# Kernel optimization log

Hardware: AMD Instinct MI355X
Metric: run time of the kernel (lower is better)

Reference implementation:

```python
import jax, jax.numpy as jnp
import numpy as np

B, CHAR_LEN, LSTM, VOCAB, NATTN = 4096, 64, 400, 73, 10

def _lstm_cell(x, h, c, W_ih, W_hh, b):
    # gates: [B, 4*LSTM] in (i, f, g, o) order, matching torch.nn.LSTMCell
    g = x @ W_ih.T + h @ W_hh.T + b
    i, f, gg, o = jnp.split(g, 4, axis=1)
    i = jax.nn.sigmoid(i); f = jax.nn.sigmoid(f)
    gg = jnp.tanh(gg); o = jax.nn.sigmoid(o)
    c_new = f * c + i * gg
    h_new = o * jnp.tanh(c_new)
    return h_new, c_new

def setup_inputs() -> dict:
    key = jax.random.key(0)
    ks = jax.random.split(key, 24)
    d = {}
    d['inputs'] = jax.random.normal(ks[0], (B, 3), jnp.float32)
    for n, k in zip(['h1','c1','h2','c2','h3','c3'], ks[1:7]):
        d[n] = jax.random.normal(k, (B, LSTM), jnp.float32) * 0.1
    d['kappa'] = jax.random.uniform(ks[7], (B, NATTN), jnp.float32) * 5.0
    d['w_prev'] = jax.random.uniform(ks[8], (B, VOCAB), jnp.float32)
    d['attention_values'] = jax.random.uniform(ks[9], (B, CHAR_LEN, VOCAB), jnp.float32)
    d['attention_lengths'] = jax.random.randint(ks[10], (B,), 1, CHAR_LEN + 1, jnp.int32)
    s = 0.05
    in1 = VOCAB + 3              # lstm1 input: [w, inputs]
    in23 = 3 + LSTM + VOCAB      # lstm2/3 input: [inputs, h, w]
    attn_in = VOCAB + 3 + LSTM
    d['W_ih1'] = jax.random.normal(ks[11], (4 * LSTM, in1), jnp.float32) * s
    d['W_hh1'] = jax.random.normal(ks[12], (4 * LSTM, LSTM), jnp.float32) * s
    d['b1'] = jax.random.normal(ks[13], (4 * LSTM,), jnp.float32) * s
    d['W_attn'] = jax.random.normal(ks[14], (3 * NATTN, attn_in), jnp.float32) * s
    d['b_attn'] = jax.random.normal(ks[15], (3 * NATTN,), jnp.float32) * s
    d['W_ih2'] = jax.random.normal(ks[16], (4 * LSTM, in23), jnp.float32) * s
    d['W_hh2'] = jax.random.normal(ks[17], (4 * LSTM, LSTM), jnp.float32) * s
    d['b2'] = jax.random.normal(ks[18], (4 * LSTM,), jnp.float32) * s
    d['W_ih3'] = jax.random.normal(ks[19], (4 * LSTM, in23), jnp.float32) * s
    d['W_hh3'] = jax.random.normal(ks[20], (4 * LSTM, LSTM), jnp.float32) * s
    d['b3'] = jax.random.normal(ks[21], (4 * LSTM,), jnp.float32) * s
    return d

def reference(inputs, h1, c1, h2, c2, h3, c3, kappa, w_prev, attention_values,
              attention_lengths, W_ih1, W_hh1, b1, W_attn, b_attn,
              W_ih2, W_hh2, b2, W_ih3, W_hh3, b3):
    char_len = attention_values.shape[1]
    # --- LSTM 1 ---
    s1_in = jnp.concatenate([w_prev, inputs], axis=1)
    h1n, c1n = _lstm_cell(s1_in, h1, c1, W_ih1, W_hh1, b1)
    # --- Gaussian-mixture location attention ---
    attn_in = jnp.concatenate([w_prev, inputs, h1n], axis=1)
    attn_params = jax.nn.softplus(attn_in @ W_attn.T + b_attn)
    alpha, beta, kap = jnp.split(attn_params, 3, axis=1)
    kap = kappa + kap / 25.0
    beta = jnp.maximum(beta, 0.01)
    u = jnp.arange(char_len, dtype=jnp.float32)[None, None, :]           # [1,1,C]
    phi = jnp.sum(alpha[:, :, None] *
                  jnp.exp(-jnp.square(kap[:, :, None] - u) / beta[:, :, None]),
                  axis=1)                                                 # [B,C]
    seq_mask = (jnp.arange(char_len)[None, :] < attention_lengths[:, None]).astype(jnp.float32)
    w = jnp.einsum('bc,bcv->bv', phi * seq_mask, attention_values)        # [B,V]
    # --- LSTM 2 & 3 ---
    s2_in = jnp.concatenate([inputs, h1n, w], axis=1)
    h2n, c2n = _lstm_cell(s2_in, h2, c2, W_ih2, W_hh2, b2)
    s3_in = jnp.concatenate([inputs, h2n, w], axis=1)
    h3n, c3n = _lstm_cell(s3_in, h3, c3, W_ih3, W_hh3, b3)
    return h3n
```

## Files before the change

kernel.cpp:

```cpp
#include <hip/hip_runtime.h>
#include <hip/hip_bf16.h>


#define B_SZ     4096
#define LSTM_N   400
#define NG       1600
#define VOCAB    73
#define NATTN    10
#define CHARLEN  64
#define KP1      512
#define KP23     896

typedef _Float16 half8 __attribute__((ext_vector_type(8)));
typedef __attribute__((ext_vector_type(4))) float floatx4;

__device__ __forceinline__ void gload_lds16(const void* g, void* l) {
    __builtin_amdgcn_global_load_lds(
        (const __attribute__((address_space(1))) void*)g,
        (__attribute__((address_space(3))) void*)l, 16, 0, 0);
}

__device__ __forceinline__ int lds_off(int r, int g) {
    return (r << 6) + ((((g ^ r) & 7)) << 3);
}

__global__ __launch_bounds__(256) void pack_wall(const float* __restrict__ Wih1,
                                                 const float* __restrict__ Whh1,
                                                 const float* __restrict__ Wih2,
                                                 const float* __restrict__ Whh2,
                                                 const float* __restrict__ Wih3,
                                                 const float* __restrict__ Whh3,
                                                 const float* __restrict__ W_attn,
                                                 _Float16* __restrict__ W1,
                                                 _Float16* __restrict__ W2,
                                                 _Float16* __restrict__ W3,
                                                 _Float16* __restrict__ Wa)
{
    const int z = blockIdx.z;
    const int n = blockIdx.y;
    const int k = blockIdx.x * 256 + threadIdx.x;
    if (z == 3) {
        if (n >= 64 || k >= KP1) return;
        float v = (n < 30 && k < 476) ? W_attn[(size_t)n * 476 + k] : 0.f;
        Wa[(size_t)n * KP1 + k] = (_Float16)v;
        return;
    }
    if (n >= NG) return;
    const int u = n >> 2, g = n & 3;
    const int src = g * 400 + u;
    if (z == 0) {
        if (k >= KP1) return;
        float v = 0.f;
        if (k < 76)           v = Wih1[(size_t)src * 76 + k];
        else if (k < 476)     v = Whh1[(size_t)src * 400 + (k - 76)];
        W1[(size_t)n * KP1 + k] = (_Float16)v;
    } else {
        if (k >= KP23) return;
        const float* Wih = (z == 1) ? Wih2 : Wih3;
        const float* Whh = (z == 1) ? Whh2 : Whh3;
        float v = 0.f;
        if (k < 476)          v = Wih[(size_t)src * 476 + k];
        else if (k < 876)     v = Whh[(size_t)src * 400 + (k - 476)];
        ((z == 1) ? W2 : W3)[(size_t)n * KP23 + k] = (_Float16)v;
    }
}

__global__ __launch_bounds__(256) void pack_x(const float* __restrict__ w_prev,
                                              const float* __restrict__ inputs,
                                              const float* __restrict__ h1,
                                              const float* __restrict__ h2,
                                              const float* __restrict__ h3,
                                              _Float16* __restrict__ X1,
                                              _Float16* __restrict__ XA,
                                              _Float16* __restrict__ X2,
                                              _Float16* __restrict__ X3)
{
    const int b = blockIdx.y;
    const int k = blockIdx.x * 256 + threadIdx.x;
    if (k < KP1) {
        float v = 0.f;
        if (k < 73)        v = w_prev[(size_t)b * 73 + k];
        else if (k < 76)   v = inputs[(size_t)b * 3 + (k - 73)];
        else if (k < 476)  v = h1[(size_t)b * 400 + (k - 76)];
        X1[(size_t)b * KP1 + k] = (_Float16)v;
        if (k < 76 || k >= 476) XA[(size_t)b * KP1 + k] = (_Float16)v;
    }
    const int kk = k - KP1;
    if (kk >= 0 && kk < KP23) {
        if (kk >= 3 && kk < 476) return;
        float v2 = 0.f, v3 = 0.f;
        if (kk < 3) { v2 = inputs[(size_t)b * 3 + kk]; v3 = v2; }
        else if (kk >= 476 && kk < 876) {
            v2 = h2[(size_t)b * 400 + (kk - 476)];
            v3 = h3[(size_t)b * 400 + (kk - 476)];
        }
        X2[(size_t)b * KP23 + kk] = (_Float16)v2;
        X3[(size_t)b * KP23 + kk] = (_Float16)v3;
    }
}

__global__ __launch_bounds__(256) void gemm_fused(const _Float16* __restrict__ Wm,
                                                  const _Float16* __restrict__ X,
                                                  const float* __restrict__ bias,
                                                  const float* __restrict__ c_in,
                                                  _Float16* __restrict__ d1, int ld1,
                                                  _Float16* __restrict__ d2, int ld2,
                                                  float* __restrict__ fout, int Kp)
{
    __shared__ _Float16 As[64 * 64];
    __shared__ _Float16 Bs[128 * 64];

    const int t    = threadIdx.x;
    const int w    = t >> 6;
    const int lane = t & 63;
    const int quad = lane >> 4;
    const int l16  = lane & 15;
    const int m0   = blockIdx.y * 64;
    const int n0   = blockIdx.x * 128;
    const int wm   = (w >> 1) * 32;
    const int wn   = (w & 1) * 64;
    const int lr   = lane >> 3;
    const int gq   = (lane & 7) ^ lr;

    floatx4 acc[2][4] = {};

    for (int k0 = 0; k0 < Kp; k0 += 64) {
        __syncthreads();
        {
            const int cr = w * 16;
#pragma unroll
            for (int s = 0; s < 2; s++)
                gload_lds16(Wm + (size_t)(m0 + cr + s * 8 + lr) * Kp + k0 + gq * 8,
                            As + (cr + s * 8) * 64);
        }
#pragma unroll
        for (int j = 0; j < 2; j++) {
            const int cr = (j * 4 + w) * 16;
#pragma unroll
            for (int s = 0; s < 2; s++)
                gload_lds16(X + (size_t)(n0 + cr + s * 8 + lr) * Kp + k0 + gq * 8,
                            Bs + (cr + s * 8) * 64);
        }
        asm volatile("s_waitcnt vmcnt(0)" ::: "memory");
        __syncthreads();

#pragma unroll
        for (int h = 0; h < 2; h++) {
            half8 af[2], bf[4];
#pragma unroll
            for (int i = 0; i < 2; i++)
                af[i] = *(const half8*)(As + lds_off(wm + i * 16 + l16, h * 4 + quad));
#pragma unroll
            for (int i = 0; i < 4; i++)
                bf[i] = *(const half8*)(Bs + lds_off(wn + i * 16 + l16, h * 4 + quad));
#pragma unroll
            for (int mt = 0; mt < 2; mt++)
#pragma unroll
                for (int nt = 0; nt < 4; nt++)
                    acc[mt][nt] = __builtin_amdgcn_mfma_f32_16x16x32_f16(
                        af[mt], bf[nt], acc[mt][nt], 0, 0, 0);
        }
    }

#pragma unroll
    for (int mt = 0; mt < 2; mt++) {
        const int u = ((m0 + wm + mt * 16) >> 2) + quad;
        const float bi  = bias[u];
        const float bff = bias[400 + u];
        const float bg  = bias[800 + u];
        const float bo  = bias[1200 + u];
#pragma unroll
        for (int nt = 0; nt < 4; nt++) {
            const int b = n0 + wn + nt * 16 + l16;
            float gi = acc[mt][nt][0] + bi;
            float gf = acc[mt][nt][1] + bff;
            float gg = acc[mt][nt][2] + bg;
            float go = acc[mt][nt][3] + bo;
            float si = 1.f / (1.f + expf(-gi));
            float sf = 1.f / (1.f + expf(-gf));
            float so = 1.f / (1.f + expf(-go));
            float cn = sf * c_in[(size_t)b * LSTM_N + u] + si * tanhf(gg);
            float h  = so * tanhf(cn);
            if (fout) {
                fout[(size_t)b * LSTM_N + u] = h;
            } else {
                _Float16 hh = (_Float16)h;
                d1[(size_t)b * ld1 + u] = hh;
                if (d2) d2[(size_t)b * ld2 + u] = hh;
            }
        }
    }
}

__global__ __launch_bounds__(256) void gemm_plain(const _Float16* __restrict__ Wa,
                                                  const _Float16* __restrict__ XA,
                                                  const float* __restrict__ bias,
                                                  float* __restrict__ C, int Kp)
{
    __shared__ _Float16 As[64 * 64];
    __shared__ _Float16 Bs[128 * 64];

    const int t    = threadIdx.x;
    const int w    = t >> 6;
    const int lane = t & 63;
    const int quad = lane >> 4;
    const int l16  = lane & 15;
    const int n0   = blockIdx.x * 128;
    const int wm   = (w >> 1) * 32;
    const int wn   = (w & 1) * 64;
    const int lr   = lane >> 3;
    const int gq   = (lane & 7) ^ lr;

    floatx4 acc[2][4] = {};

    for (int k0 = 0; k0 < Kp; k0 += 64) {
        __syncthreads();
        {
            const int cr = w * 16;
#pragma unroll
            for (int s = 0; s < 2; s++)
                gload_lds16(Wa + (size_t)(cr + s * 8 + lr) * Kp + k0 + gq * 8,
                            As + (cr + s * 8) * 64);
        }
#pragma unroll
        for (int j = 0; j < 2; j++) {
            const int cr = (j * 4 + w) * 16;
#pragma unroll
            for (int s = 0; s < 2; s++)
                gload_lds16(XA + (size_t)(n0 + cr + s * 8 + lr) * Kp + k0 + gq * 8,
                            Bs + (cr + s * 8) * 64);
        }
        asm volatile("s_waitcnt vmcnt(0)" ::: "memory");
        __syncthreads();

#pragma unroll
        for (int h = 0; h < 2; h++) {
            half8 af[2], bf[4];
#pragma unroll
            for (int i = 0; i < 2; i++)
                af[i] = *(const half8*)(As + lds_off(wm + i * 16 + l16, h * 4 + quad));
#pragma unroll
            for (int i = 0; i < 4; i++)
                bf[i] = *(const half8*)(Bs + lds_off(wn + i * 16 + l16, h * 4 + quad));
#pragma unroll
            for (int mt = 0; mt < 2; mt++)
#pragma unroll
                for (int nt = 0; nt < 4; nt++)
                    acc[mt][nt] = __builtin_amdgcn_mfma_f32_16x16x32_f16(
                        af[mt], bf[nt], acc[mt][nt], 0, 0, 0);
        }
    }

#pragma unroll
    for (int mt = 0; mt < 2; mt++) {
#pragma unroll
        for (int r = 0; r < 4; r++) {
            const int m = wm + mt * 16 + quad * 4 + r;
            if (m >= 30) continue;
            const float bv = bias[m];
#pragma unroll
            for (int nt = 0; nt < 4; nt++) {
                const int b = n0 + wn + nt * 16 + l16;
                C[(size_t)b * 32 + m] = acc[mt][nt][r] + bv;
            }
        }
    }
}

__global__ __launch_bounds__(256) void attn_phi(const float* __restrict__ AP,
                                                const float* __restrict__ kappa,
                                                const float* __restrict__ AV,
                                                const int* __restrict__ alen,
                                                _Float16* __restrict__ X2,
                                                _Float16* __restrict__ X3)
{
    __shared__ float prm[4][32];
    __shared__ float phi_s[4][CHARLEN];

    const int t = threadIdx.x;
    const int wave = t >> 6;
    const int lane = t & 63;
    const int b = blockIdx.x * 4 + wave;

    if (lane < 30) {
        float p  = AP[(size_t)b * 32 + lane];
        float sp = (p > 20.f) ? p : log1pf(expf(p));
        float v;
        if (lane < 10)      v = sp;
        else if (lane < 20) v = fmaxf(sp, 0.01f);
        else                v = kappa[(size_t)b * NATTN + (lane - 20)] + sp * (1.f / 25.f);
        prm[wave][lane] = v;
    }
    __syncthreads();

    const int len = alen[b];
    {
        int c = lane;
        float phi = 0.f;
#pragma unroll
        for (int j = 0; j < NATTN; j++) {
            float d = prm[wave][20 + j] - (float)c;
            phi += prm[wave][j] * expf(-d * d / prm[wave][10 + j]);
        }
        phi_s[wave][c] = (c < len) ? phi : 0.f;
    }
    __syncthreads();

    for (int v0 = 0; v0 < VOCAB; v0 += 64) {
        const int v = v0 + lane;
        if (v < VOCAB) {
            const float* avb = AV + (size_t)b * CHARLEN * VOCAB + v;
            float s = 0.f;
            for (int c = 0; c < len; c++)
                s += phi_s[wave][c] * avb[(size_t)c * VOCAB];
            _Float16 wv = (_Float16)s;
            X2[(size_t)b * KP23 + 403 + v] = wv;
            X3[(size_t)b * KP23 + 403 + v] = wv;
        }
    }
}

extern "C" void kernel_launch(void* const* d_in, const int* in_sizes, int n_in,
                              void* d_out, int out_size, void* d_ws, size_t ws_size,
                              hipStream_t stream)
{
    const float* inputs = (const float*)d_in[0];
    const float* h1     = (const float*)d_in[1];
    const float* c1     = (const float*)d_in[2];
    const float* h2     = (const float*)d_in[3];
    const float* c2     = (const float*)d_in[4];
    const float* h3     = (const float*)d_in[5];
    const float* c3     = (const float*)d_in[6];
    const float* kappa  = (const float*)d_in[7];
    const float* w_prev = (const float*)d_in[8];
    const float* AV     = (const float*)d_in[9];
    const int*   alen   = (const int*)d_in[10];
    const float* W_ih1  = (const float*)d_in[11];
    const float* W_hh1  = (const float*)d_in[12];
    const float* b1     = (const float*)d_in[13];
    const float* W_attn = (const float*)d_in[14];
    const float* b_attn = (const float*)d_in[15];
    const float* W_ih2  = (const float*)d_in[16];
    const float* W_hh2  = (const float*)d_in[17];
    const float* b2     = (const float*)d_in[18];
    const float* W_ih3  = (const float*)d_in[19];
    const float* W_hh3  = (const float*)d_in[20];
    const float* b3     = (const float*)d_in[21];
    float* out = (float*)d_out;

    char* p = (char*)d_ws;
    _Float16* X1 = (_Float16*)p; p += (size_t)B_SZ * KP1 * 2;
    _Float16* XA = (_Float16*)p; p += (size_t)B_SZ * KP1 * 2;
    _Float16* X2 = (_Float16*)p; p += (size_t)B_SZ * KP23 * 2;
    _Float16* X3 = (_Float16*)p; p += (size_t)B_SZ * KP23 * 2;
    _Float16* W1 = (_Float16*)p; p += (size_t)NG * KP1 * 2;
    _Float16* W2 = (_Float16*)p; p += (size_t)NG * KP23 * 2;
    _Float16* W3 = (_Float16*)p; p += (size_t)NG * KP23 * 2;
    _Float16* Wa = (_Float16*)p; p += (size_t)64 * KP1 * 2;
    float* AP = (float*)p;

    pack_wall<<<dim3(4, NG, 4), 256, 0, stream>>>(W_ih1, W_hh1, W_ih2, W_hh2,
                                                  W_ih3, W_hh3, W_attn,
                                                  W1, W2, W3, Wa);
    pack_x<<<dim3((KP1 + KP23 + 255) / 256, B_SZ), 256, 0, stream>>>(
        w_prev, inputs, h1, h2, h3, X1, XA, X2, X3);

    const dim3 fgrid(B_SZ / 128, NG / 64);

    gemm_fused<<<fgrid, 256, 0, stream>>>(W1, X1, b1, c1,
                                          XA + 76, KP1, X2 + 3, KP23, nullptr, KP1);
    gemm_plain<<<dim3(B_SZ / 128, 1), 256, 0, stream>>>(Wa, XA, b_attn, AP, KP1);
    attn_phi<<<B_SZ / 4, 256, 0, stream>>>(AP, kappa, AV, alen, X2, X3);
    gemm_fused<<<fgrid, 256, 0, stream>>>(W2, X2, b2, c2,
                                          X3 + 3, KP23, nullptr, 0, nullptr, KP23);
    gemm_fused<<<fgrid, 256, 0, stream>>>(W3, X3, b3, c3,
                                          nullptr, 0, nullptr, 0, out, KP23);
}
```

Before: 297.4 us.

## Use 2-wave GEMM blocks with 64x64 warp tiles and vectorize pack kernels

The fused LSTM GEMM now runs with 128 threads (2 waves) per block instead of 4. Each wave computes a 64x64 tile (4x4 MFMA fragments), which raises register-level reuse of the A and B fragments. The weight and activation pack kernels are rewritten to handle four elements per thread with float4 loads and half4 stores. The trade-off is fewer waves per block and more accumulators per wave, which may reduce latency hiding and occupancy. There is also a risk of misaligned float4 reads for rows of 76 or 476 floats: 76*4 and 476*4 bytes are 16-byte multiples, but offset k-76 may not be.

New measurement: 299.8 us. Within noise of the previous version (+0.8%).

```diff
diff --git a/kernel.cpp b/kernel.cpp
--- a/kernel.cpp
+++ b/kernel.cpp
@@ -12,6 +12,7 @@
 #define KP23     896
 
 typedef _Float16 half8 __attribute__((ext_vector_type(8)));
+typedef _Float16 half4 __attribute__((ext_vector_type(4)));
 typedef __attribute__((ext_vector_type(4))) float floatx4;
 
 __device__ __forceinline__ void gload_lds16(const void* g, void* l) {
@@ -21,7 +22,7 @@
 }
 
 __device__ __forceinline__ int lds_off(int r, int g) {
-    return (r << 6) + ((((g ^ r) & 7)) << 3);
+    return (r << 6) + (((g ^ r) & 7) << 3);
 }
 
 __global__ __launch_bounds__(256) void pack_wall(const float* __restrict__ Wih1,
@@ -38,30 +39,33 @@
 {
     const int z = blockIdx.z;
     const int n = blockIdx.y;
-    const int k = blockIdx.x * 256 + threadIdx.x;
+    const int c = threadIdx.x;
+    float4 v = make_float4(0.f, 0.f, 0.f, 0.f);
     if (z == 3) {
-        if (n >= 64 || k >= KP1) return;
-        float v = (n < 30 && k < 476) ? W_attn[(size_t)n * 476 + k] : 0.f;
-        Wa[(size_t)n * KP1 + k] = (_Float16)v;
+        if (n >= 64 || c >= KP1 / 4) return;
+        if (n < 30 && 4 * c < 476) v = *(const float4*)(W_attn + (size_t)n * 476 + 4 * c);
+        half4 h = { (_Float16)v.x, (_Float16)v.y, (_Float16)v.z, (_Float16)v.w };
+        *(half4*)(Wa + (size_t)n * KP1 + 4 * c) = h;
         return;
     }
-    if (n >= NG) return;
     const int u = n >> 2, g = n & 3;
     const int src = g * 400 + u;
     if (z == 0) {
-        if (k >= KP1) return;
-        float v = 0.f;
-        if (k < 76)           v = Wih1[(size_t)src * 76 + k];
-        else if (k < 476)     v = Whh1[(size_t)src * 400 + (k - 76)];
-        W1[(size_t)n * KP1 + k] = (_Float16)v;
+        if (c >= KP1 / 4) return;
+        const int k = 4 * c;
+        if (k < 76)           v = *(const float4*)(Wih1 + (size_t)src * 76 + k);
+        else if (k < 476)     v = *(const float4*)(Whh1 + (size_t)src * 400 + (k - 76));
+        half4 h = { (_Float16)v.x, (_Float16)v.y, (_Float16)v.z, (_Float16)v.w };
+        *(half4*)(W1 + (size_t)n * KP1 + k) = h;
     } else {
-        if (k >= KP23) return;
+        if (c >= KP23 / 4) return;
+        const int k = 4 * c;
         const float* Wih = (z == 1) ? Wih2 : Wih3;
         const float* Whh = (z == 1) ? Whh2 : Whh3;
-        float v = 0.f;
-        if (k < 476)          v = Wih[(size_t)src * 476 + k];
-        else if (k < 876)     v = Whh[(size_t)src * 400 + (k - 476)];
-        ((z == 1) ? W2 : W3)[(size_t)n * KP23 + k] = (_Float16)v;
+        if (k < 476)          v = *(const float4*)(Wih + (size_t)src * 476 + k);
+        else if (k < 876)     v = *(const float4*)(Whh + (size_t)src * 400 + (k - 476));
+        half4 h = { (_Float16)v.x, (_Float16)v.y, (_Float16)v.z, (_Float16)v.w };
+        *(half4*)(((z == 1) ? W2 : W3) + (size_t)n * KP23 + k) = h;
     }
 }
 
@@ -76,30 +80,45 @@
                                               _Float16* __restrict__ X3)
 {
     const int b = blockIdx.y;
-    const int k = blockIdx.x * 256 + threadIdx.x;
-    if (k < KP1) {
-        float v = 0.f;
-        if (k < 73)        v = w_prev[(size_t)b * 73 + k];
-        else if (k < 76)   v = inputs[(size_t)b * 3 + (k - 73)];
-        else if (k < 476)  v = h1[(size_t)b * 400 + (k - 76)];
-        X1[(size_t)b * KP1 + k] = (_Float16)v;
-        if (k < 76 || k >= 476) XA[(size_t)b * KP1 + k] = (_Float16)v;
-    }
-    const int kk = k - KP1;
-    if (kk >= 0 && kk < KP23) {
-        if (kk >= 3 && kk < 476) return;
-        float v2 = 0.f, v3 = 0.f;
-        if (kk < 3) { v2 = inputs[(size_t)b * 3 + kk]; v3 = v2; }
-        else if (kk >= 476 && kk < 876) {
-            v2 = h2[(size_t)b * 400 + (kk - 476)];
-            v3 = h3[(size_t)b * 400 + (kk - 476)];
-        }
-        X2[(size_t)b * KP23 + kk] = (_Float16)v2;
-        X3[(size_t)b * KP23 + kk] = (_Float16)v3;
-    }
-}
-
-__global__ __launch_bounds__(256) void gemm_fused(const _Float16* __restrict__ Wm,
+    const int c = blockIdx.x * 256 + threadIdx.x;
+    if (c < KP1 / 4) {
+        float v[4];
+#pragma unroll
+        for (int j = 0; j < 4; j++) {
+            const int k = 4 * c + j;
+            float x = 0.f;
+            if (k < 73)        x = w_prev[(size_t)b * 73 + k];
+            else if (k < 76)   x = inputs[(size_t)b * 3 + (k - 73)];
+            else if (k < 476)  x = h1[(size_t)b * 400 + (k - 76)];
+            v[j] = x;
+        }
+        half4 h = { (_Float16)v[0], (_Float16)v[1], (_Float16)v[2], (_Float16)v[3] };
+        *(half4*)(X1 + (size_t)b * KP1 + 4 * c) = h;
+        if (c < 19 || c > 118) *(half4*)(XA + (size_t)b * KP1 + 4 * c) = h;
+        return;
+    }
+    const int cc = c - KP1 / 4;
+    if (cc >= KP23 / 4) return;
+    if (cc >= 1 && cc <= 118) return;
+    float v2[4], v3[4];
+#pragma unroll
+    for (int j = 0; j < 4; j++) {
+        const int k = 4 * cc + j;
+        float a = 0.f, bq = 0.f;
+        if (k < 3) { a = inputs[(size_t)b * 3 + k]; bq = a; }
+        else if (k >= 476 && k < 876) {
+            a  = h2[(size_t)b * 400 + (k - 476)];
+            bq = h3[(size_t)b * 400 + (k - 476)];
+        }
+        v2[j] = a; v3[j] = bq;
+    }
+    half4 g2 = { (_Float16)v2[0], (_Float16)v2[1], (_Float16)v2[2], (_Float16)v2[3] };
+    half4 g3 = { (_Float16)v3[0], (_Float16)v3[1], (_Float16)v3[2], (_Float16)v3[3] };
+    *(half4*)(X2 + (size_t)b * KP23 + 4 * cc) = g2;
+    *(half4*)(X3 + (size_t)b * KP23 + 4 * cc) = g3;
+}
+
+__global__ __launch_bounds__(128) void gemm_fused(const _Float16* __restrict__ Wm,
                                                   const _Float16* __restrict__ X,
                                                   const float* __restrict__ bias,
                                                   const float* __restrict__ c_in,
@@ -117,44 +136,37 @@
     const int l16  = lane & 15;
     const int m0   = blockIdx.y * 64;
     const int n0   = blockIdx.x * 128;
-    const int wm   = (w >> 1) * 32;
-    const int wn   = (w & 1) * 64;
+    const int wn   = w * 64;
     const int lr   = lane >> 3;
     const int gq   = (lane & 7) ^ lr;
 
-    floatx4 acc[2][4] = {};
+    floatx4 acc[4][4] = {};
 
     for (int k0 = 0; k0 < Kp; k0 += 64) {
         __syncthreads();
-        {
-            const int cr = w * 16;
-#pragma unroll
-            for (int s = 0; s < 2; s++)
-                gload_lds16(Wm + (size_t)(m0 + cr + s * 8 + lr) * Kp + k0 + gq * 8,
-                            As + (cr + s * 8) * 64);
-        }
-#pragma unroll
-        for (int j = 0; j < 2; j++) {
-            const int cr = (j * 4 + w) * 16;
-#pragma unroll
-            for (int s = 0; s < 2; s++)
-                gload_lds16(X + (size_t)(n0 + cr + s * 8 + lr) * Kp + k0 + gq * 8,
-                            Bs + (cr + s * 8) * 64);
+#pragma unroll
+        for (int s = 0; s < 4; s++) {
+            const int cr = w * 32 + s * 8;
+            gload_lds16(Wm + (size_t)(m0 + cr + lr) * Kp + k0 + gq * 8, As + cr * 64);
+        }
+#pragma unroll
+        for (int s = 0; s < 8; s++) {
+            const int cr = w * 64 + s * 8;
+            gload_lds16(X + (size_t)(n0 + cr + lr) * Kp + k0 + gq * 8, Bs + cr * 64);
         }
         asm volatile("s_waitcnt vmcnt(0)" ::: "memory");
         __syncthreads();
 
 #pragma unroll
         for (int h = 0; h < 2; h++) {
-            half8 af[2], bf[4];
-#pragma unroll
-            for (int i = 0; i < 2; i++)
-                af[i] = *(const half8*)(As + lds_off(wm + i * 16 + l16, h * 4 + quad));
-#pragma unroll
-            for (int i = 0; i < 4; i++)
+            half8 af[4], bf[4];
+#pragma unroll
+            for (int i = 0; i < 4; i++) {
+                af[i] = *(const half8*)(As + lds_off(i * 16 + l16, h * 4 + quad));
                 bf[i] = *(const half8*)(Bs + lds_off(wn + i * 16 + l16, h * 4 + quad));
-#pragma unroll
-            for (int mt = 0; mt < 2; mt++)
+            }
+#pragma unroll
+            for (int mt = 0; mt < 4; mt++)
 #pragma unroll
                 for (int nt = 0; nt < 4; nt++)
                     acc[mt][nt] = __builtin_amdgcn_mfma_f32_16x16x32_f16(
@@ -163,8 +175,8 @@
     }
 
 #pragma unroll
-    for (int mt = 0; mt < 2; mt++) {
-        const int u = ((m0 + wm + mt * 16) >> 2) + quad;
+    for (int mt = 0; mt < 4; mt++) {
+        const int u = (m0 >> 2) + mt * 4 + quad;
         const float bi  = bias[u];
         const float bff = bias[400 + u];
         const float bg  = bias[800 + u];
@@ -359,20 +371,20 @@
     _Float16* Wa = (_Float16*)p; p += (size_t)64 * KP1 * 2;
     float* AP = (float*)p;
 
-    pack_wall<<<dim3(4, NG, 4), 256, 0, stream>>>(W_ih1, W_hh1, W_ih2, W_hh2,
+    pack_wall<<<dim3(1, NG, 4), 256, 0, stream>>>(W_ih1, W_hh1, W_ih2, W_hh2,
                                                   W_ih3, W_hh3, W_attn,
                                                   W1, W2, W3, Wa);
-    pack_x<<<dim3((KP1 + KP23 + 255) / 256, B_SZ), 256, 0, stream>>>(
-        w_prev, inputs, h1, h2, h3, X1, XA, X2, X3);
+    pack_x<<<dim3(2, B_SZ), 256, 0, stream>>>(w_prev, inputs, h1, h2, h3,
+                                              X1, XA, X2, X3);
 
     const dim3 fgrid(B_SZ / 128, NG / 64);
 
-    gemm_fused<<<fgrid, 256, 0, stream>>>(W1, X1, b1, c1,
+    gemm_fused<<<fgrid, 128, 0, stream>>>(W1, X1, b1, c1,
                                           XA + 76, KP1, X2 + 3, KP23, nullptr, KP1);
     gemm_plain<<<dim3(B_SZ / 128, 1), 256, 0, stream>>>(Wa, XA, b_attn, AP, KP1);
     attn_phi<<<B_SZ / 4, 256, 0, stream>>>(AP, kappa, AV, alen, X2, X3);
-    gemm_fused<<<fgrid, 256, 0, stream>>>(W2, X2, b2, c2,
+    gemm_fused<<<fgrid, 128, 0, stream>>>(W2, X2, b2, c2,
                                           X3 + 3, KP23, nullptr, 0, nullptr, KP23);
-    gemm_fused<<<fgrid, 256, 0, stream>>>(W3, X3, b3, c3,
+    gemm_fused<<<fgrid, 128, 0, stream>>>(W3, X3, b3, c3,
                                           nullptr, 0, nullptr, 0, out, KP23);
 }
```
